# Kernel tuning notes

Measured on AMD Instinct MI355X. Metric: run time of the kernel, lower is better.

Reference implementation:

```python
import jax, jax.numpy as jnp
import numpy as np

# 8 trilerp corners in (x, y, z) component order, matching the original's
# [floor/ceil] enumeration: fff, ffc, fcf, fcc, cff, cfc, ccf, ccc.
CORNERS = np.array([[0, 0, 0], [0, 0, 1], [0, 1, 0], [0, 1, 1],
                    [1, 0, 0], [1, 0, 1], [1, 1, 0], [1, 1, 1]], dtype=np.int32)

N = 32768          # number of points
NUM_KERNELS = 4    # submodels
GRID = 16          # voxel grid size
C_IN = 64          # input_channels
C_OUT = 64         # features


def setup_inputs() -> dict:
    key = jax.random.key(0)
    k1, k2, k3, k4, k5 = jax.random.split(key, 5)
    param_idxs = jax.random.randint(k1, (N, 1), 0, NUM_KERNELS, dtype=jnp.int32)
    pos = jax.random.uniform(k2, (N, 3), dtype=jnp.float32)
    xs = jax.random.normal(k3, (N, C_IN), dtype=jnp.float32)
    # he_uniform over fan_in = input_channels
    limit = np.sqrt(6.0 / C_IN).astype(np.float32)
    kernels = jax.random.uniform(
        k4, (NUM_KERNELS, GRID, GRID, GRID, C_IN, C_OUT),
        dtype=jnp.float32, minval=-limit, maxval=limit)
    biases = jnp.zeros((NUM_KERNELS, GRID, GRID, GRID, C_OUT), dtype=jnp.float32)
    return {"param_idxs": param_idxs, "pos": pos, "xs": xs,
            "kernels": kernels, "biases": biases}


def reference(param_idxs, pos, xs, kernels, biases):
    """Trilinearly-interpolated per-point dense layer.

    Equivalent to building kernel = sum_c w_c * K_c and computing x @ kernel + bias;
    by linearity we accumulate w_c * (x @ K_c + b_c) directly, avoiding the
    materialized per-point interpolated kernel.
    """
    grid = kernels.shape[1]
    pidx = param_idxs.reshape(-1)            # (N,)
    loc = pos * grid - 0.5                    # (N, 3)
    floored = jnp.floor(loc)
    ceil_w = loc - floored                    # trilerp weights toward ceil
    floor_w = 1.0 - ceil_w
    out = jnp.zeros((pos.shape[0], kernels.shape[-1]), dtype=xs.dtype)
    for corner in CORNERS:                    # fixed 8-iteration loop
        idx = jnp.clip((floored + corner).astype(jnp.int32), 0, grid - 1)  # (N,3)
        w = jnp.prod(jnp.where(corner[None, :] == 1, ceil_w, floor_w), axis=-1)  # (N,)
        # Original indexes kernels[pidx, z, y, x] with z=idx[:,2], y=idx[:,1], x=idx[:,0]
        gk = kernels[pidx, idx[:, 2], idx[:, 1], idx[:, 0]]  # (N, C_in, C_out)
        gb = biases[pidx, idx[:, 2], idx[:, 1], idx[:, 0]]   # (N, C_out)
        out = out + w[:, None] * (jnp.einsum('nc,ncf->nf', xs, gk) + gb)
    return out
```

## Files before the change

### kernel.cpp

```cpp
#include <hip/hip_runtime.h>
#include <math.h>

#define NPTS   32768
#define NK     4
#define GRIDN  16
#define CIN    64
#define COUT   64
#define NCELLS (NK*GRIDN*GRIDN*GRIDN)
#define CAP    128
#define KPAD   68

typedef __attribute__((ext_vector_type(8))) short  short8;
typedef __attribute__((ext_vector_type(4))) float  f32x4;

static __device__ inline unsigned short f2bf(float f) {
    unsigned int u = __builtin_bit_cast(unsigned int, f);
    unsigned int r = u + 0x7fff + ((u >> 16) & 1);
    return (unsigned short)(r >> 16);
}

__global__ void k_scatter(const int* __restrict__ pidx, const float* __restrict__ pos,
                          int* __restrict__ cnt, int2* __restrict__ ent,
                          float* __restrict__ out, int out_elems,
                          int n, int cap) {
    int t = blockIdx.x * blockDim.x + threadIdx.x;

    {
        int o = t * 8;
        if (o + 8 <= out_elems) {
            float4 z = {0.f, 0.f, 0.f, 0.f};
            *(float4*)&out[o + 0] = z;
            *(float4*)&out[o + 4] = z;
        }
    }

    int p = t >> 3;
    if (p >= n) return;
    int c  = t & 7;
    int pk = pidx[p];
    float lx = pos[3*p+0]*16.f - 0.5f;
    float ly = pos[3*p+1]*16.f - 0.5f;
    float lz = pos[3*p+2]*16.f - 0.5f;
    float flx = floorf(lx), fly = floorf(ly), flz = floorf(lz);
    float tx = lx - flx, ty = ly - fly, tz = lz - flz;
    int fx = (int)flx, fy = (int)fly, fz = (int)flz;
    int c0 = c & 1, c1 = (c >> 1) & 1, c2 = (c >> 2) & 1;
    int ix = min(max(fx + c0, 0), GRIDN-1);
    int iy = min(max(fy + c1, 0), GRIDN-1);
    int iz = min(max(fz + c2, 0), GRIDN-1);
    float w = (c0 ? tx : 1.f - tx) * (c1 ? ty : 1.f - ty) * (c2 ? tz : 1.f - tz);
    int cell = ((pk*GRIDN + iz)*GRIDN + iy)*GRIDN + ix;
    int e = atomicAdd(&cnt[cell], 1);
    if (e < cap) ent[(size_t)cell * cap + e] = make_int2(p, __float_as_int(w));
}

__global__ __launch_bounds__(256)
void k_main(const float* __restrict__ xs, const float* __restrict__ kernels,
            const float* __restrict__ biases, const int* __restrict__ cnt,
            const int2* __restrict__ ent, float* __restrict__ out, int cap) {
    __shared__ unsigned short Ks[4][CIN * KPAD];

    int tid  = threadIdx.x;
    int wv   = tid >> 6;
    int l    = tid & 63;
    int q    = l >> 4;
    int m    = l & 15;
    int cell = blockIdx.x * 4 + wv;

    int count = min(cnt[cell], cap);
    if (count == 0) return;

    const float* Kg = kernels + (size_t)cell * (CIN * COUT);
    unsigned short* ks = &Ks[wv][0];
#pragma unroll
    for (int it = 0; it < 16; ++it) {
        int e   = it * 256 + l * 4;
        float4 kv = *(const float4*)&Kg[e];
        int row = e >> 6, col = e & 63;
        ushort4 kb = { f2bf(kv.x), f2bf(kv.y), f2bf(kv.z), f2bf(kv.w) };
        *(ushort4*)&ks[row * KPAD + col] = kb;
    }

    short8 Bf[4][2];
#pragma unroll
    for (int c = 0; c < 4; ++c)
#pragma unroll
        for (int s = 0; s < 2; ++s)
#pragma unroll
            for (int j = 0; j < 8; ++j)
                Bf[c][s][j] = (short)ks[(s*32 + q*8 + j) * KPAD + c*16 + m];

    float bias_c[4];
#pragma unroll
    for (int c = 0; c < 4; ++c)
        bias_c[c] = biases[(size_t)cell * COUT + c*16 + m];

    const int2* eb = ent + (size_t)cell * cap;
    int nb = (count + 15) >> 4;
    for (int b = 0; b < nb; ++b) {
        int r0 = b << 4;
        int2 em = (r0 + m < count) ? eb[r0 + m] : make_int2(0, 0);
        int apid = em.x;

        short8 af[2];
#pragma unroll
        for (int s = 0; s < 2; ++s) {
            const float4 x0 = *(const float4*)&xs[(size_t)apid*CIN + s*32 + q*8 + 0];
            const float4 x1 = *(const float4*)&xs[(size_t)apid*CIN + s*32 + q*8 + 4];
            af[s][0] = (short)f2bf(x0.x); af[s][1] = (short)f2bf(x0.y);
            af[s][2] = (short)f2bf(x0.z); af[s][3] = (short)f2bf(x0.w);
            af[s][4] = (short)f2bf(x1.x); af[s][5] = (short)f2bf(x1.y);
            af[s][6] = (short)f2bf(x1.z); af[s][7] = (short)f2bf(x1.w);
        }

        f32x4 acc[4];
#pragma unroll
        for (int c = 0; c < 4; ++c) acc[c] = (f32x4){0.f, 0.f, 0.f, 0.f};
#pragma unroll
        for (int s = 0; s < 2; ++s)
#pragma unroll
            for (int c = 0; c < 4; ++c)
                acc[c] = __builtin_amdgcn_mfma_f32_16x16x32_bf16(af[s], Bf[c][s], acc[c], 0, 0, 0);

#pragma unroll
        for (int reg = 0; reg < 4; ++reg) {
            int   r     = q*4 + reg;
            int   pid_r = __shfl(em.x, r);
            float w_r   = __shfl(__int_as_float(em.y), r);
            if (w_r != 0.f) {
                float* orow = out + (size_t)pid_r * COUT + m;
#pragma unroll
                for (int c = 0; c < 4; ++c)
                    unsafeAtomicAdd(&orow[c*16], w_r * (acc[c][reg] + bias_c[c]));
            }
        }
    }
}

extern "C" void kernel_launch(void* const* d_in, const int* in_sizes, int n_in,
                              void* d_out, int out_size, void* d_ws, size_t ws_size,
                              hipStream_t stream) {
    const int*   pidx    = (const int*)  d_in[0];
    const float* pos     = (const float*)d_in[1];
    const float* xs      = (const float*)d_in[2];
    const float* kernels = (const float*)d_in[3];
    const float* biases  = (const float*)d_in[4];
    float*       out     = (float*)d_out;
    int n = in_sizes[0];

    int*  cnt = (int*)d_ws;
    int2* ent = (int2*)((char*)d_ws + (size_t)NCELLS * sizeof(int));

    int cap = CAP;
    size_t avail = (ws_size > (size_t)NCELLS * sizeof(int))
                 ? (ws_size - (size_t)NCELLS * sizeof(int)) / (sizeof(int2) * NCELLS)
                 : 0;
    if ((size_t)cap > avail) cap = (int)avail;

    hipMemsetAsync(cnt, 0, NCELLS * sizeof(int), stream);

    int eblocks = (n * 8 + 255) / 256;
    k_scatter<<<eblocks, 256, 0, stream>>>(pidx, pos, cnt, ent, out, out_size, n, cap);
    k_main  <<<NCELLS/4, 256, 0, stream>>>(xs, kernels, biases, cnt, ent, out, cap);
}
```

Measured before the change: 398.9 us.

## Fuse memset, scatter and cell GEMM into one cooperative persistent kernel

Replaces the memset plus two-kernel sequence with a single cooperative kernel. It zeroes counters and output, scatters point-corner entries, and runs the per-cell MFMA pass, with grid-wide syncs between the phases. Cells are walked in a persistent grid-stride loop, one wave per cell. The kernel tile is now loaded straight from global memory into registers with strided scalar loads instead of being staged through LDS, which removes shared memory but makes the global reads less coalesced. This saves launch and memset overhead but adds grid-sync cost and limits the grid to the occupancy that can be resident at once.

```diff
diff --git a/kernel.cpp b/kernel.cpp
--- a/kernel.cpp
+++ b/kernel.cpp
@@ -1,5 +1,8 @@
 #include <hip/hip_runtime.h>
+#include <hip/hip_cooperative_groups.h>
 #include <math.h>
+
+namespace cg = cooperative_groups;
 
 #define NPTS   32768
 #define NK     4
@@ -8,7 +11,6 @@
 #define COUT   64
 #define NCELLS (NK*GRIDN*GRIDN*GRIDN)
 #define CAP    128
-#define KPAD   68
 
 typedef __attribute__((ext_vector_type(8))) short  short8;
 typedef __attribute__((ext_vector_type(4))) float  f32x4;
@@ -17,6 +19,116 @@
     unsigned int u = __builtin_bit_cast(unsigned int, f);
     unsigned int r = u + 0x7fff + ((u >> 16) & 1);
     return (unsigned short)(r >> 16);
+}
+
+__global__ __launch_bounds__(256, 4)
+void k_fused(const int* __restrict__ pidx, const float* __restrict__ pos,
+             const float* __restrict__ xs, const float* __restrict__ kernels,
+             const float* __restrict__ biases, int* __restrict__ cnt,
+             int2* __restrict__ ent, float* __restrict__ out,
+             int out_elems, int n, int cap) {
+    cg::grid_group grid = cg::this_grid();
+    int T  = gridDim.x * blockDim.x;
+    int t0 = blockIdx.x * blockDim.x + threadIdx.x;
+
+    for (int i = t0; i < NCELLS; i += T) cnt[i] = 0;
+    {
+        float4 z = {0.f, 0.f, 0.f, 0.f};
+        int nv = out_elems >> 2;
+        for (int i = t0; i < nv; i += T) *(float4*)&out[i << 2] = z;
+    }
+    __threadfence();
+    grid.sync();
+
+    int items = n * 8;
+    for (int it = t0; it < items; it += T) {
+        int p  = it >> 3;
+        int c  = it & 7;
+        int pk = pidx[p];
+        float lx = pos[3*p+0]*16.f - 0.5f;
+        float ly = pos[3*p+1]*16.f - 0.5f;
+        float lz = pos[3*p+2]*16.f - 0.5f;
+        float flx = floorf(lx), fly = floorf(ly), flz = floorf(lz);
+        float tx = lx - flx, ty = ly - fly, tz = lz - flz;
+        int fx = (int)flx, fy = (int)fly, fz = (int)flz;
+        int c0 = c & 1, c1 = (c >> 1) & 1, c2 = (c >> 2) & 1;
+        int ix = min(max(fx + c0, 0), GRIDN-1);
+        int iy = min(max(fy + c1, 0), GRIDN-1);
+        int iz = min(max(fz + c2, 0), GRIDN-1);
+        float w = (c0 ? tx : 1.f - tx) * (c1 ? ty : 1.f - ty) * (c2 ? tz : 1.f - tz);
+        int cell = ((pk*GRIDN + iz)*GRIDN + iy)*GRIDN + ix;
+        int e = atomicAdd(&cnt[cell], 1);
+        if (e < cap) ent[(size_t)cell * cap + e] = make_int2(p, __float_as_int(w));
+    }
+    __threadfence();
+    grid.sync();
+
+    int l  = t0 & 63;
+    int gw = t0 >> 6;
+    int nw = T >> 6;
+    int q  = l >> 4;
+    int m  = l & 15;
+
+    for (int cell = gw; cell < NCELLS; cell += nw) {
+        int count = min(cnt[cell], cap);
+        if (count == 0) continue;
+
+        const float* Kg = kernels + (size_t)cell * (CIN * COUT);
+        short8 Bf[4][2];
+#pragma unroll
+        for (int c = 0; c < 4; ++c)
+#pragma unroll
+            for (int s = 0; s < 2; ++s)
+#pragma unroll
+                for (int j = 0; j < 8; ++j)
+                    Bf[c][s][j] = (short)f2bf(Kg[(s*32 + q*8 + j)*COUT + c*16 + m]);
+
+        float bias_c[4];
+#pragma unroll
+        for (int c = 0; c < 4; ++c)
+            bias_c[c] = biases[(size_t)cell * COUT + c*16 + m];
+
+        const int2* eb = ent + (size_t)cell * cap;
+        int nb = (count + 15) >> 4;
+        for (int b = 0; b < nb; ++b) {
+            int r0 = b << 4;
+            int2 em = (r0 + m < count) ? eb[r0 + m] : make_int2(0, 0);
+            int apid = em.x;
+
+            short8 af[2];
+#pragma unroll
+            for (int s = 0; s < 2; ++s) {
+                const float4 x0 = *(const float4*)&xs[(size_t)apid*CIN + s*32 + q*8 + 0];
+                const float4 x1 = *(const float4*)&xs[(size_t)apid*CIN + s*32 + q*8 + 4];
+                af[s][0] = (short)f2bf(x0.x); af[s][1] = (short)f2bf(x0.y);
+                af[s][2] = (short)f2bf(x0.z); af[s][3] = (short)f2bf(x0.w);
+                af[s][4] = (short)f2bf(x1.x); af[s][5] = (short)f2bf(x1.y);
+                af[s][6] = (short)f2bf(x1.z); af[s][7] = (short)f2bf(x1.w);
+            }
+
+            f32x4 acc[4];
+#pragma unroll
+            for (int c = 0; c < 4; ++c) acc[c] = (f32x4){0.f, 0.f, 0.f, 0.f};
+#pragma unroll
+            for (int s = 0; s < 2; ++s)
+#pragma unroll
+                for (int c = 0; c < 4; ++c)
+                    acc[c] = __builtin_amdgcn_mfma_f32_16x16x32_bf16(af[s], Bf[c][s], acc[c], 0, 0, 0);
+
+#pragma unroll
+            for (int reg = 0; reg < 4; ++reg) {
+                int   r     = q*4 + reg;
+                int   pid_r = __shfl(em.x, r);
+                float w_r   = __shfl(__int_as_float(em.y), r);
+                if (w_r != 0.f) {
+                    float* orow = out + (size_t)pid_r * COUT + m;
+#pragma unroll
+                    for (int c = 0; c < 4; ++c)
+                        unsafeAtomicAdd(&orow[c*16], w_r * (acc[c][reg] + bias_c[c]));
+                }
+            }
+        }
+    }
 }
 
 __global__ void k_scatter(const int* __restrict__ pidx, const float* __restrict__ pos,
@@ -24,7 +136,6 @@
                           float* __restrict__ out, int out_elems,
                           int n, int cap) {
     int t = blockIdx.x * blockDim.x + threadIdx.x;
-
     {
         int o = t * 8;
         if (o + 8 <= out_elems) {
@@ -33,7 +144,6 @@
             *(float4*)&out[o + 4] = z;
         }
     }
-
     int p = t >> 3;
     if (p >= n) return;
     int c  = t & 7;
@@ -58,8 +168,6 @@
 void k_main(const float* __restrict__ xs, const float* __restrict__ kernels,
             const float* __restrict__ biases, const int* __restrict__ cnt,
             const int2* __restrict__ ent, float* __restrict__ out, int cap) {
-    __shared__ unsigned short Ks[4][CIN * KPAD];
-
     int tid  = threadIdx.x;
     int wv   = tid >> 6;
     int l    = tid & 63;
@@ -71,16 +179,6 @@
     if (count == 0) return;
 
     const float* Kg = kernels + (size_t)cell * (CIN * COUT);
-    unsigned short* ks = &Ks[wv][0];
-#pragma unroll
-    for (int it = 0; it < 16; ++it) {
-        int e   = it * 256 + l * 4;
-        float4 kv = *(const float4*)&Kg[e];
-        int row = e >> 6, col = e & 63;
-        ushort4 kb = { f2bf(kv.x), f2bf(kv.y), f2bf(kv.z), f2bf(kv.w) };
-        *(ushort4*)&ks[row * KPAD + col] = kb;
-    }
-
     short8 Bf[4][2];
 #pragma unroll
     for (int c = 0; c < 4; ++c)
@@ -88,7 +186,7 @@
         for (int s = 0; s < 2; ++s)
 #pragma unroll
             for (int j = 0; j < 8; ++j)
-                Bf[c][s][j] = (short)ks[(s*32 + q*8 + j) * KPAD + c*16 + m];
+                Bf[c][s][j] = (short)f2bf(Kg[(s*32 + q*8 + j)*COUT + c*16 + m]);
 
     float bias_c[4];
 #pragma unroll
@@ -147,6 +245,7 @@
     const float* biases  = (const float*)d_in[4];
     float*       out     = (float*)d_out;
     int n = in_sizes[0];
+    int out_elems = out_size;
 
     int*  cnt = (int*)d_ws;
     int2* ent = (int2*)((char*)d_ws + (size_t)NCELLS * sizeof(int));
@@ -157,9 +256,32 @@
                  : 0;
     if ((size_t)cap > avail) cap = (int)avail;
 
+    static int s_blocks = 0;
+    static int s_coop_ok = -1;
+    if (s_blocks == 0) {
+        int occ = 0;
+        hipError_t e = hipOccupancyMaxActiveBlocksPerMultiprocessor(
+            &occ, (const void*)k_fused, 256, 0);
+        if (e != hipSuccess || occ < 1) occ = 4;
+        long b = (long)occ * 256;
+        if (b > 4096) b = 4096;
+        if (b < 256)  b = 256;
+        s_blocks = (int)b;
+    }
+
+    if (s_coop_ok != 0) {
+        void* args[] = { (void*)&pidx, (void*)&pos, (void*)&xs, (void*)&kernels,
+                         (void*)&biases, (void*)&cnt, (void*)&ent, (void*)&out,
+                         (void*)&out_elems, (void*)&n, (void*)&cap };
+        hipError_t e = hipLaunchCooperativeKernel((const void*)k_fused,
+                                                  dim3(s_blocks), dim3(256),
+                                                  args, 0, stream);
+        if (e == hipSuccess) { s_coop_ok = 1; return; }
+        s_coop_ok = 0;
+    }
+
     hipMemsetAsync(cnt, 0, NCELLS * sizeof(int), stream);
-
     int eblocks = (n * 8 + 255) / 256;
-    k_scatter<<<eblocks, 256, 0, stream>>>(pidx, pos, cnt, ent, out, out_size, n, cap);
+    k_scatter<<<eblocks, 256, 0, stream>>>(pidx, pos, cnt, ent, out, out_elems, n, cap);
     k_main  <<<NCELLS/4, 256, 0, stream>>>(xs, kernels, biases, cnt, ent, out, cap);
 }
```

After: 635.1 us. +59.2%, slower.

## Assign one block per cell with each wave owning a 16-column output slice

Applied to the files above, without the earlier changes.

Switches from four cells per block (one wave per cell, covering all 64 outputs) to one cell per block, where each of the four waves computes a 16-wide slice of the output columns. Kernel tiles are now loaded straight from global memory into registers, so the shared-memory staging is gone, and the entry index for the next batch is prefetched one iteration ahead. This spreads each cell's work over four waves and cuts per-wave register and LDS use. In exchange, every wave reloads and re-converts the same xs rows, and there are four times as many blocks, many of which exit early on empty cells.

```diff
diff --git a/kernel.cpp b/kernel.cpp
--- a/kernel.cpp
+++ b/kernel.cpp
@@ -8,7 +8,6 @@
 #define COUT   64
 #define NCELLS (NK*GRIDN*GRIDN*GRIDN)
 #define CAP    128
-#define KPAD   68
 
 typedef __attribute__((ext_vector_type(8))) short  short8;
 typedef __attribute__((ext_vector_type(4))) float  f32x4;
@@ -24,7 +23,6 @@
                           float* __restrict__ out, int out_elems,
                           int n, int cap) {
     int t = blockIdx.x * blockDim.x + threadIdx.x;
-
     {
         int o = t * 8;
         if (o + 8 <= out_elems) {
@@ -33,7 +31,6 @@
             *(float4*)&out[o + 4] = z;
         }
     }
-
     int p = t >> 3;
     if (p >= n) return;
     int c  = t & 7;
@@ -58,48 +55,35 @@
 void k_main(const float* __restrict__ xs, const float* __restrict__ kernels,
             const float* __restrict__ biases, const int* __restrict__ cnt,
             const int2* __restrict__ ent, float* __restrict__ out, int cap) {
-    __shared__ unsigned short Ks[4][CIN * KPAD];
-
     int tid  = threadIdx.x;
     int wv   = tid >> 6;
     int l    = tid & 63;
     int q    = l >> 4;
     int m    = l & 15;
-    int cell = blockIdx.x * 4 + wv;
+    int cell = blockIdx.x;
 
     int count = min(cnt[cell], cap);
     if (count == 0) return;
+    const int2* eb = ent + (size_t)cell * cap;
+
+    int2 em = (m < count) ? eb[m] : make_int2(0, 0);
 
     const float* Kg = kernels + (size_t)cell * (CIN * COUT);
-    unsigned short* ks = &Ks[wv][0];
+    short8 Bf[2];
 #pragma unroll
-    for (int it = 0; it < 16; ++it) {
-        int e   = it * 256 + l * 4;
-        float4 kv = *(const float4*)&Kg[e];
-        int row = e >> 6, col = e & 63;
-        ushort4 kb = { f2bf(kv.x), f2bf(kv.y), f2bf(kv.z), f2bf(kv.w) };
-        *(ushort4*)&ks[row * KPAD + col] = kb;
-    }
+    for (int s = 0; s < 2; ++s)
+#pragma unroll
+        for (int j = 0; j < 8; ++j)
+            Bf[s][j] = (short)f2bf(Kg[(s*32 + q*8 + j)*COUT + wv*16 + m]);
 
-    short8 Bf[4][2];
-#pragma unroll
-    for (int c = 0; c < 4; ++c)
-#pragma unroll
-        for (int s = 0; s < 2; ++s)
-#pragma unroll
-            for (int j = 0; j < 8; ++j)
-                Bf[c][s][j] = (short)ks[(s*32 + q*8 + j) * KPAD + c*16 + m];
+    float bias_c = biases[(size_t)cell * COUT + wv*16 + m];
 
-    float bias_c[4];
-#pragma unroll
-    for (int c = 0; c < 4; ++c)
-        bias_c[c] = biases[(size_t)cell * COUT + c*16 + m];
-
-    const int2* eb = ent + (size_t)cell * cap;
     int nb = (count + 15) >> 4;
     for (int b = 0; b < nb; ++b) {
         int r0 = b << 4;
-        int2 em = (r0 + m < count) ? eb[r0 + m] : make_int2(0, 0);
+        int2 em_n = make_int2(0, 0);
+        if (b + 1 < nb && r0 + 16 + m < count) em_n = eb[r0 + 16 + m];
+
         int apid = em.x;
 
         short8 af[2];
@@ -113,14 +97,10 @@
             af[s][6] = (short)f2bf(x1.z); af[s][7] = (short)f2bf(x1.w);
         }
 
-        f32x4 acc[4];
-#pragma unroll
-        for (int c = 0; c < 4; ++c) acc[c] = (f32x4){0.f, 0.f, 0.f, 0.f};
+        f32x4 acc = {0.f, 0.f, 0.f, 0.f};
 #pragma unroll
         for (int s = 0; s < 2; ++s)
-#pragma unroll
-            for (int c = 0; c < 4; ++c)
-                acc[c] = __builtin_amdgcn_mfma_f32_16x16x32_bf16(af[s], Bf[c][s], acc[c], 0, 0, 0);
+            acc = __builtin_amdgcn_mfma_f32_16x16x32_bf16(af[s], Bf[s], acc, 0, 0, 0);
 
 #pragma unroll
         for (int reg = 0; reg < 4; ++reg) {
@@ -128,12 +108,11 @@
             int   pid_r = __shfl(em.x, r);
             float w_r   = __shfl(__int_as_float(em.y), r);
             if (w_r != 0.f) {
-                float* orow = out + (size_t)pid_r * COUT + m;
-#pragma unroll
-                for (int c = 0; c < 4; ++c)
-                    unsafeAtomicAdd(&orow[c*16], w_r * (acc[c][reg] + bias_c[c]));
+                unsafeAtomicAdd(&out[(size_t)pid_r * COUT + wv*16 + m],
+                                w_r * (acc[reg] + bias_c));
             }
         }
+        em = em_n;
     }
 }
 
@@ -161,5 +140,5 @@
 
     int eblocks = (n * 8 + 255) / 256;
     k_scatter<<<eblocks, 256, 0, stream>>>(pidx, pos, cnt, ent, out, out_size, n, cap);
-    k_main  <<<NCELLS/4, 256, 0, stream>>>(xs, kernels, biases, cnt, ent, out, cap);
+    k_main  <<<NCELLS, 256, 0, stream>>>(xs, kernels, biases, cnt, ent, out, cap);
 }
```

Measured after the change: 390.0 us. 1.02x faster.
